# Kernel tuning notes

Hardware: AMD Instinct MI355X
Metric: run time of the kernel (lower is better)

Reference implementation:

```python
import jax, jax.numpy as jnp
import numpy as np

N_NODES = 65536   # entity nodes across batched docs
N_EDGES = 32768   # edges per etype
D_CTX = 768       # PTM hidden size ('n' feature)
D_REL = 97        # relation_num (out_feature)
CHUNK = 1024      # edge chunk for the per-edge bilinear


def setup_inputs() -> dict:
    key = jax.random.key(0)
    ks = jax.random.split(key, 10)
    n = jax.random.normal(ks[0], (N_NODES, D_CTX), jnp.float32)
    e_inter = jax.random.normal(ks[1], (N_EDGES, D_REL), jnp.float32)
    e_intra = jax.random.normal(ks[2], (N_EDGES, D_REL), jnp.float32)
    # nn.Bilinear(768, 97, 1, bias=False): weight [1, 768, 97]
    W_bl = jax.random.normal(ks[3], (1, D_CTX, D_REL), jnp.float32) * 0.02
    # nn.Bilinear(194, 194, 97): weight [97, 194, 194], bias [97]
    W_bl1 = jax.random.normal(ks[4], (D_REL, 2 * D_REL, 2 * D_REL), jnp.float32) * 0.02
    b_bl1 = jnp.zeros((D_REL,), jnp.float32)
    src_inter = jax.random.randint(ks[5], (N_EDGES,), 0, N_NODES, jnp.int32)
    dst_inter = jax.random.randint(ks[6], (N_EDGES,), 0, N_NODES, jnp.int32)
    src_intra = jax.random.randint(ks[7], (N_EDGES,), 0, N_NODES, jnp.int32)
    dst_intra = jax.random.randint(ks[8], (N_EDGES,), 0, N_NODES, jnp.int32)
    return {"n": n, "e_inter": e_inter, "e_intra": e_intra,
            "W_bl": W_bl, "W_bl1": W_bl1, "b_bl1": b_bl1,
            "src_inter": src_inter, "dst_inter": dst_inter,
            "src_intra": src_intra, "dst_intra": dst_intra}


def reference(n, e_inter, e_intra, W_bl, W_bl1, b_bl1,
              src_inter, dst_inter, src_intra, dst_intra):
    num_nodes = n.shape[0]
    # node_reduce: score = bilinear(n[dst], e) -> softmax over incoming edges
    # bl(src_n, e) = n[dst] @ W_bl[0] @ e  (precompute node projection once)
    proj = n @ W_bl[0]                                  # [N, D_REL]

    def node_reduce(e, dst):
        s = jnp.sum(proj[dst] * e, axis=-1)             # per-edge score [E]
        smax = jax.ops.segment_max(s, dst, num_segments=num_nodes)
        ex = jnp.exp(s - smax[dst])
        denom = jax.ops.segment_sum(ex, dst, num_segments=num_nodes)
        alpha = ex / denom[dst]                          # segment softmax
        # attention-weighted sum of mailbox messages -> [N, D_REL]
        return jax.ops.segment_sum(e * alpha[:, None], dst, num_segments=num_nodes)

    # multi_update_all(..., 'stack') over etypes ['inter','intra'] then flatten
    rel = jnp.concatenate([node_reduce(e_inter, dst_inter),
                           node_reduce(e_intra, dst_intra)], axis=-1)  # [N, 194]

    def edge_gate(e, src, dst):
        s_rel = rel[src]                                 # [E, 194]
        d_rel = rel[dst]                                 # [E, 194]
        d_in = s_rel.shape[1]

        def f(args):
            s, d = args                                  # [CHUNK, 194]
            return jnp.einsum('ei,kij,ej->ek', s, W_bl1, d, optimize=True) + b_bl1

        gate = jax.lax.map(f, (s_rel.reshape(-1, CHUNK, d_in),
                               d_rel.reshape(-1, CHUNK, d_in)))
        gate = gate.reshape(e.shape[0], -1)              # [E, D_REL]
        return e + jax.nn.sigmoid(gate) * e

    out_inter = edge_gate(e_inter, src_inter, dst_inter)
    out_intra = edge_gate(e_intra, src_intra, dst_intra)
    return jnp.stack([out_inter, out_intra])             # [2, E, D_REL]
```

## Files before the change

kernel.cpp:

```cpp
#include <hip/hip_runtime.h>
#include <hip/hip_bf16.h>
#include <stdint.h>


typedef __attribute__((ext_vector_type(8))) short short8;
typedef __attribute__((ext_vector_type(4))) float f32x4;
typedef _Float16 half8 __attribute__((ext_vector_type(8)));

#define NN 65536
#define NE1 32768
#define NEG 65536
#define DC 768
#define DR 97
#define DR2 194
#define RELSTR 200
#define RELHS 400
#define KI 194
#define KS 7
#define NT 7
#define EPB 64
#define SSTR 200
#define PSTR 72
#define NDESC_G 4160

#define OFF_REL   0ull
#define OFF_BPK   52428800ull
#define OFF_IDX   62164992ull
#define OFF_SMAX  62427136ull
#define OFF_DEN   62951424ull
#define OFF_META  63475712ull
#define OFF_DESC  63475968ull
#define OFF_WPK   63542528ull

static __device__ __forceinline__ unsigned fkey(float f) {
    unsigned b = __float_as_uint(f);
    return (b & 0x80000000u) ? ~b : (b | 0x80000000u);
}
static __device__ __forceinline__ float funkey(unsigned k) {
    return __uint_as_float((k & 0x80000000u) ? (k & 0x7fffffffu) : ~k);
}
static __device__ __forceinline__ unsigned pk2(_Float16 a, _Float16 b) {
    union { _Float16 h[2]; unsigned u; } x;
    x.h[0] = a; x.h[1] = b;
    return x.u;
}
static __device__ __forceinline__ int nstate(bool zi, bool zx) {
    return zi ? (zx ? 3 : 2) : (zx ? 1 : 0);
}
static __device__ __forceinline__ int nsplit_of(int b) { (void)b; return 4; }
static __device__ __forceinline__ int kindbase_of(int b) { return (b % 3) * 4; }

__global__ void build_bpk(const float* __restrict__ W, half8* __restrict__ Bpk) {
    int id = blockIdx.x * blockDim.x + threadIdx.x;
    const int total = KI * KS * NT * 64;
    if (id >= total) return;
    int l = id & 63;
    int g = id >> 6;
    int t = g % NT;
    int ks = (g / NT) % KS;
    int i = g / (NT * KS);
    int kk = t * 16 + (l & 15);
    int jb = ks * 32 + (l >> 4) * 8;
    half8 pk;
#pragma unroll
    for (int m = 0; m < 8; ++m) {
        int j = jb + m;
        float f = (kk < DR && j < DR2) ? W[(size_t)kk * (DR2 * DR2) + i * DR2 + j] : 0.f;
        pk[m] = (_Float16)f;
    }
    Bpk[id] = pk;
}

__global__ void build_wpk(const float* __restrict__ Wb, half8* __restrict__ Wpk) {
    int id = blockIdx.x * blockDim.x + threadIdx.x;
    const int total = 24 * NT * 64;
    if (id >= total) return;
    int l = id & 63;
    int g = id >> 6;
    int t = g % NT;
    int k2 = g / NT;
    int col = t * 16 + (l & 15);
    int j0 = k2 * 32 + (l >> 4) * 8;
    half8 pk;
#pragma unroll
    for (int m = 0; m < 8; ++m) {
        float f = (col < DR) ? Wb[(size_t)(j0 + m) * DR + col] : 0.f;
        pk[m] = (_Float16)f;
    }
    Wpk[id] = pk;
}

__launch_bounds__(512, 8)
__global__ void proj_mfma(const float* __restrict__ nmat, const half8* __restrict__ Wpk,
                          float* __restrict__ proj) {
    __shared__ __align__(16) _Float16 a_lds[128][PSTR];
    int tid = threadIdx.x;
    int r0 = blockIdx.x << 7;
    int w = tid >> 6, lane = tid & 63;
    int er = (w << 4) + (lane & 15);
    int lk = lane >> 4;

    f32x4 acc[NT];
#pragma unroll
    for (int t = 0; t < NT; ++t) acc[t] = (f32x4){0.f, 0.f, 0.f, 0.f};

    int srow = tid >> 2;
    int sc0 = (tid & 3) << 4;
    const float* nrow = nmat + (size_t)(r0 + srow) * DC + sc0;

    for (int k0 = 0; k0 < DC; k0 += 64) {
        __syncthreads();
        {
            const f32x4* p = (const f32x4*)(nrow + k0);
            _Float16* dst = &a_lds[srow][sc0];
#pragma unroll
            for (int q = 0; q < 4; ++q) {
                f32x4 v = p[q];
                *(unsigned*)&dst[q * 4]     = pk2((_Float16)v[0], (_Float16)v[1]);
                *(unsigned*)&dst[q * 4 + 2] = pk2((_Float16)v[2], (_Float16)v[3]);
            }
        }
        __syncthreads();
#pragma unroll
        for (int kk = 0; kk < 2; ++kk) {
            half8 af = *(const half8*)&a_lds[er][kk * 32 + lk * 8];
            const half8* bp = Wpk + (size_t)((k0 >> 5) + kk) * (NT * 64) + lane;
#pragma unroll
            for (int t = 0; t < NT; ++t)
                acc[t] = __builtin_amdgcn_mfma_f32_16x16x32_f16(af, bp[t * 64], acc[t], 0, 0, 0);
        }
    }

#pragma unroll
    for (int t = 0; t < NT; ++t) {
        int col = t * 16 + (lane & 15);
        if (col < DR) {
#pragma unroll
            for (int r = 0; r < 4; ++r) {
                int row = r0 + (w << 4) + lk * 4 + r;
                proj[(size_t)row * DR + col] = acc[t][r];
            }
        }
    }
}

__global__ void score_kernel(const float* __restrict__ proj,
                             const float* __restrict__ e_inter, const float* __restrict__ e_intra,
                             const int* __restrict__ dst_inter, const int* __restrict__ dst_intra,
                             float* __restrict__ s_buf, unsigned* __restrict__ smax_key) {
    int wid = (blockIdx.x * blockDim.x + threadIdx.x) >> 6;
    int lane = threadIdx.x & 63;
    if (wid >= NEG) return;
    int et = wid >> 15, le = wid & (NE1 - 1);
    const float* e = (et ? e_intra : e_inter) + (size_t)le * DR;
    int dst = (et ? dst_intra : dst_inter)[le];
    const float* pr = proj + (size_t)dst * DR;
    float p = pr[lane] * e[lane];
    if (lane < DR - 64) p += pr[lane + 64] * e[lane + 64];
#pragma unroll
    for (int off = 32; off > 0; off >>= 1) p += __shfl_down(p, off);
    if (lane == 0) {
        s_buf[wid] = p;
        atomicMax(&smax_key[et * NN + dst], fkey(p));
    }
}

__global__ void accum_kernel(const float* __restrict__ s_buf,
                             const float* __restrict__ e_inter, const float* __restrict__ e_intra,
                             const int* __restrict__ dst_inter, const int* __restrict__ dst_intra,
                             const unsigned* __restrict__ smax_key,
                             float* __restrict__ denom, float* __restrict__ rel) {
    int wid = (blockIdx.x * blockDim.x + threadIdx.x) >> 6;
    int lane = threadIdx.x & 63;
    if (wid >= NEG) return;
    int et = wid >> 15, le = wid & (NE1 - 1);
    const float* e = (et ? e_intra : e_inter) + (size_t)le * DR;
    int dst = (et ? dst_intra : dst_inter)[le];
    float s = s_buf[wid];
    float mx = funkey(smax_key[et * NN + dst]);
    float ex = __expf(s - mx);
    if (lane == 0) atomicAdd(&denom[et * NN + dst], ex);
    float* rrow = rel + (size_t)dst * RELSTR + et * DR;
    atomicAdd(&rrow[lane], e[lane] * ex);
    if (lane < DR - 64) atomicAdd(&rrow[lane + 64], e[lane + 64] * ex);
}

__global__ void dinv_kernel(float* __restrict__ denom) {
    int i = blockIdx.x * blockDim.x + threadIdx.x;
    if (i < 2 * NN) {
        float d = denom[i];
        denom[i] = (d > 0.f) ? (1.f / d) : 0.f;
    }
}

__global__ void pack_kernel(float* __restrict__ relf, const float* __restrict__ dinv) {
    int n = blockIdx.x * blockDim.x + threadIdx.x;
    if (n >= NN) return;
    float di0 = dinv[n], di1 = dinv[NN + n];
    unsigned* row = (unsigned*)(relf + (size_t)n * RELSTR);
#pragma unroll 10
    for (int q = 0; q < 50; ++q) {
        uint4 v = *(const uint4*)(row + q * 4);
        int c = q * 4;
        _Float16 h0 = (_Float16)(__uint_as_float(v.x) * ((c + 0 < DR) ? di0 : di1));
        _Float16 h1 = (_Float16)(__uint_as_float(v.y) * ((c + 1 < DR) ? di0 : di1));
        _Float16 h2 = (_Float16)(__uint_as_float(v.z) * ((c + 2 < DR) ? di0 : di1));
        _Float16 h3 = (_Float16)(__uint_as_float(v.w) * ((c + 3 < DR) ? di0 : di1));
        uint2 o;
        o.x = pk2(h0, h1);
        o.y = pk2(h2, h3);
        *(uint2*)(row + q * 2) = o;
    }
}

__global__ void classify_kernel(const float* __restrict__ dinv,
                                const int* __restrict__ src_inter, const int* __restrict__ dst_inter,
                                const int* __restrict__ src_intra, const int* __restrict__ dst_intra,
                                unsigned* __restrict__ meta) {
    __shared__ unsigned h[16];
    if (threadIdx.x < 16) h[threadIdx.x] = 0;
    __syncthreads();
    int gid = blockIdx.x * blockDim.x + threadIdx.x;
    if (gid < NEG) {
        int et = gid >> 15, le = gid & (NE1 - 1);
        int sn = (et ? src_intra : src_inter)[le];
        int dn = (et ? dst_intra : dst_inter)[le];
        int ss = nstate(dinv[sn] == 0.f, dinv[NN + sn] == 0.f);
        int ds = nstate(dinv[dn] == 0.f, dinv[NN + dn] == 0.f);
        int b = (ss == 3 || ds == 3) ? 9 : ss * 3 + ds;
        atomicAdd(&h[b], 1u);
    }
    __syncthreads();
    if (threadIdx.x < 10 && h[threadIdx.x])
        atomicAdd(&meta[threadIdx.x], h[threadIdx.x]);
}

__global__ void setup1_kernel(unsigned* __restrict__ meta) {
    if (threadIdx.x != 0 || blockIdx.x != 0) return;
    unsigned run = 0;
    for (int b = 0; b < 10; ++b) {
        meta[32 + b] = run;
        meta[16 + b] = run;
        run += meta[b];
    }
    unsigned c = 0;
    for (int b = 0; b < 9; ++b) {
        meta[52 + b] = c;
        c += ((meta[b] + EPB - 1) / EPB) * (unsigned)nsplit_of(b);
    }
    meta[48] = c;
}

__global__ void setup2_kernel(const unsigned* __restrict__ meta, uint4* __restrict__ desc) {
    int j = blockIdx.x * blockDim.x + threadIdx.x;
    if (j >= (int)meta[48]) return;
    int b = 8;
    for (int q = 1; q < 9; ++q)
        if (j < (int)meta[52 + q]) { b = q - 1; break; }
    int p = j - (int)meta[52 + b];
    int ns = nsplit_of(b);
    int ci = p / ns;
    int si = p - ci * ns;
    int cnt = (int)meta[b];
    int cbase = (int)meta[32 + b] + ci * EPB;
    int ccnt = cnt - ci * EPB;
    if (ccnt > EPB) ccnt = EPB;
    int kind = kindbase_of(b) + si;
    int sclass = b / 3;
    desc[j] = make_uint4((unsigned)kind, (unsigned)cbase, (unsigned)ccnt, (unsigned)sclass);
}

__global__ void scatter_kernel(const float* __restrict__ dinv,
                               const int* __restrict__ src_inter, const int* __restrict__ dst_inter,
                               const int* __restrict__ src_intra, const int* __restrict__ dst_intra,
                               unsigned* __restrict__ meta, int* __restrict__ idxbuf) {
    __shared__ unsigned cur[16];
    __shared__ unsigned base[16];
    if (threadIdx.x < 16) cur[threadIdx.x] = 0;
    __syncthreads();
    int gid = blockIdx.x * blockDim.x + threadIdx.x;
    int b = -1;
    unsigned r = 0;
    if (gid < NEG) {
        int et = gid >> 15, le = gid & (NE1 - 1);
        int sn = (et ? src_intra : src_inter)[le];
        int dn = (et ? dst_intra : dst_inter)[le];
        int ss = nstate(dinv[sn] == 0.f, dinv[NN + sn] == 0.f);
        int ds = nstate(dinv[dn] == 0.f, dinv[NN + dn] == 0.f);
        b = (ss == 3 || ds == 3) ? 9 : ss * 3 + ds;
        r = atomicAdd(&cur[b], 1u);
    }
    __syncthreads();
    if (threadIdx.x < 10 && cur[threadIdx.x])
        base[threadIdx.x] = atomicAdd(&meta[16 + threadIdx.x], cur[threadIdx.x]);
    __syncthreads();
    if (b >= 0) idxbuf[base[b] + r] = gid;
}

__global__ void skip_kernel(const unsigned* __restrict__ meta, const int* __restrict__ idxbuf,
                            const float* __restrict__ e_inter, const float* __restrict__ e_intra,
                            const float* __restrict__ bias, float* __restrict__ out) {
    int n9 = (int)meta[9];
    int base9 = (int)meta[41];
    int k = threadIdx.x;
    float g = 0.f;
    if (k < DR) {
        float b = bias[k];
        g = 1.f + 1.f / (1.f + __expf(-b));
    }
    for (int q = blockIdx.x; q < n9; q += gridDim.x) {
        int gid = idxbuf[base9 + q];
        int et = gid >> 15, le = gid & (NE1 - 1);
        const float* e = (et ? e_intra : e_inter) + (size_t)le * DR;
        if (k < DR) out[(size_t)gid * DR + k] = e[k] * g;
    }
}

#define GATE_BODY(KS0v, KS1v, T0v, T1v)                                        \
    {                                                                          \
        constexpr int NKSv = (KS1v) - (KS0v);                                  \
        constexpr int NTTv = (T1v) - (T0v);                                    \
        f32x4 acc0[NTTv], acc1[NTTv];                                          \
        _Pragma("unroll")                                                      \
        for (int tt = 0; tt < NTTv; ++tt) {                                    \
            acc0[tt] = (f32x4){0.f, 0.f, 0.f, 0.f};                            \
            acc1[tt] = (f32x4){0.f, 0.f, 0.f, 0.f};                            \
        }                                                                      \
        const half8* bl = Bpk + lane;                                          \
        for (int i = i0; i < iEnd; ++i) {                                      \
            _Float16 s0 = buf[er0 * SSTR + i];                                 \
            _Float16 s1 = buf[er1 * SSTR + i];                                 \
            half8 sv0 = {s0, s0, s0, s0, s0, s0, s0, s0};                      \
            half8 sv1 = {s1, s1, s1, s1, s1, s1, s1, s1};                      \
            const half8* bi = bl + (size_t)((i * KS + (KS0v)) * NT + (T0v)) * 64; \
            _Pragma("unroll")                                                  \
            for (int ks = 0; ks < NKSv; ++ks) {                                \
                half8 af0 = sv0 * dv0[(KS0v) + ks];                            \
                half8 af1 = sv1 * dv1[(KS0v) + ks];                            \
                _Pragma("unroll")                                              \
                for (int tt = 0; tt < NTTv; ++tt) {                            \
                    half8 bv = bi[(ks * NT + tt) * 64];                        \
                    acc0[tt] = __builtin_amdgcn_mfma_f32_16x16x32_f16(af0, bv, acc0[tt], 0, 0, 0); \
                    acc1[tt] = __builtin_amdgcn_mfma_f32_16x16x32_f16(af1, bv, acc1[tt], 0, 0, 0); \
                }                                                              \
            }                                                                  \
        }                                                                      \
        _Pragma("unroll")                                                      \
        for (int r = 0; r < 4; ++r) {                                          \
            int row = (w << 5) + lk * 4 + r;                                   \
            if (row < ccnt) {                                                  \
                int gid = idxbuf[cbase + row];                                 \
                int et = gid >> 15, le = gid & (NE1 - 1);                      \
                const float* e = (et ? e_intra : e_inter) + (size_t)le * DR;   \
                float* o = out + (size_t)gid * DR;                             \
                _Pragma("unroll")                                              \
                for (int tt = 0; tt < NTTv; ++tt) {                            \
                    int k = ((T0v) + tt) * 16 + (lane & 15);                   \
                    if (k < DR) {                                              \
                        float g = acc0[tt][r] + bias[k];                       \
                        float sg = 1.f / (1.f + __expf(-g));                   \
                        o[k] = e[k] * (1.f + sg);                              \
                    }                                                          \
                }                                                              \
            }                                                                  \
        }                                                                      \
        _Pragma("unroll")                                                      \
        for (int r = 0; r < 4; ++r) {                                          \
            int row = (w << 5) + 16 + lk * 4 + r;                              \
            if (row < ccnt) {                                                  \
                int gid = idxbuf[cbase + row];                                 \
                int et = gid >> 15, le = gid & (NE1 - 1);                      \
                const float* e = (et ? e_intra : e_inter) + (size_t)le * DR;   \
                float* o = out + (size_t)gid * DR;                             \
                _Pragma("unroll")                                              \
                for (int tt = 0; tt < NTTv; ++tt) {                            \
                    int k = ((T0v) + tt) * 16 + (lane & 15);                   \
                    if (k < DR) {                                              \
                        float g = acc1[tt][r] + bias[k];                       \
                        float sg = 1.f / (1.f + __expf(-g));                   \
                        o[k] = e[k] * (1.f + sg);                              \
                    }                                                          \
                }                                                              \
            }                                                                  \
        }                                                                      \
    }

__launch_bounds__(128, 4)
__global__ void gate_all(const _Float16* __restrict__ relh, const float* __restrict__ dinv,
                         const half8* __restrict__ Bpk, const float* __restrict__ bias,
                         const int* __restrict__ src_inter, const int* __restrict__ dst_inter,
                         const int* __restrict__ src_intra, const int* __restrict__ dst_intra,
                         const float* __restrict__ e_inter, const float* __restrict__ e_intra,
                         const int* __restrict__ idxbuf, const unsigned* __restrict__ meta,
                         const uint4* __restrict__ desc, float* __restrict__ out) {
    if (blockIdx.x >= meta[48]) return;
    uint4 de = desc[blockIdx.x];
    int kind = (int)de.x;
    int cbase = (int)de.y;
    int ccnt = (int)de.z;
    int sclass = (int)de.w;
    int i0 = (sclass == 2) ? DR : 0;
    int iEnd = (sclass == 0) ? DR2 : (i0 + DR);

    __shared__ __align__(16) _Float16 buf[EPB * SSTR];
    int tid = threadIdx.x;
    int w = tid >> 6;
    int lane = tid & 63;
    int lk = lane >> 4;
    int er0 = (w << 5) + (lane & 15);
    int er1 = er0 + 16;

    if (tid < EPB) {
        int edge = tid;
        int rc = cbase + ((edge < ccnt) ? edge : (ccnt - 1));
        int gid = idxbuf[rc];
        int et = gid >> 15, le = gid & (NE1 - 1);
        int dn = (et ? dst_intra : dst_inter)[le];
        const uint4* rp = (const uint4*)(relh + (size_t)dn * RELHS);
        uint4* dp = (uint4*)&buf[edge * SSTR];
#pragma unroll
        for (int q = 0; q < 25; ++q) dp[q] = rp[q];
    }
    __syncthreads();

    half8 dv0[KS], dv1[KS];
#pragma unroll
    for (int ks = 0; ks < KS; ++ks) {
        if (ks == 6 && lk > 0) {
            dv0[ks] = (half8){0, 0, 0, 0, 0, 0, 0, 0};
            dv1[ks] = (half8){0, 0, 0, 0, 0, 0, 0, 0};
        } else {
            dv0[ks] = *(const half8*)&buf[er0 * SSTR + ks * 32 + lk * 8];
            dv1[ks] = *(const half8*)&buf[er1 * SSTR + ks * 32 + lk * 8];
        }
    }
    __syncthreads();

    if (tid < EPB) {
        int edge = tid;
        int rc = cbase + ((edge < ccnt) ? edge : (ccnt - 1));
        int gid = idxbuf[rc];
        int et = gid >> 15, le = gid & (NE1 - 1);
        int sn = (et ? src_intra : src_inter)[le];
        const uint4* rp = (const uint4*)(relh + (size_t)sn * RELHS);
        uint4* dp = (uint4*)&buf[edge * SSTR];
#pragma unroll
        for (int q = 0; q < 25; ++q) dp[q] = rp[q];
    }
    __syncthreads();

    switch (kind) {
        case 0:  GATE_BODY(0, 7, 0, 2); break;
        case 1:  GATE_BODY(0, 7, 2, 4); break;
        case 2:  GATE_BODY(0, 7, 4, 6); break;
        case 3:  GATE_BODY(0, 7, 6, 7); break;
        case 4:  GATE_BODY(0, 4, 0, 2); break;
        case 5:  GATE_BODY(0, 4, 2, 4); break;
        case 6:  GATE_BODY(0, 4, 4, 6); break;
        case 7:  GATE_BODY(0, 4, 6, 7); break;
        case 8:  GATE_BODY(3, 7, 0, 2); break;
        case 9:  GATE_BODY(3, 7, 2, 4); break;
        case 10: GATE_BODY(3, 7, 4, 6); break;
        case 11: GATE_BODY(3, 7, 6, 7); break;
        default: break;
    }
}

extern "C" void kernel_launch(void* const* d_in, const int* in_sizes, int n_in,
                              void* d_out, int out_size, void* d_ws, size_t ws_size,
                              hipStream_t stream) {
    (void)in_sizes; (void)n_in; (void)out_size; (void)ws_size;
    const float* nmat     = (const float*)d_in[0];
    const float* e_inter  = (const float*)d_in[1];
    const float* e_intra  = (const float*)d_in[2];
    const float* W_bl     = (const float*)d_in[3];
    const float* W_bl1    = (const float*)d_in[4];
    const float* b_bl1    = (const float*)d_in[5];
    const int* src_inter  = (const int*)d_in[6];
    const int* dst_inter  = (const int*)d_in[7];
    const int* src_intra  = (const int*)d_in[8];
    const int* dst_intra  = (const int*)d_in[9];
    float* out = (float*)d_out;

    char* ws = (char*)d_ws;
    float* regA     = (float*)(ws + OFF_REL);
    half8* Bpk      = (half8*)(ws + OFF_BPK);
    int* idxbuf     = (int*)(ws + OFF_IDX);
    float* s_buf    = (float*)(ws + OFF_IDX);
    unsigned* smax  = (unsigned*)(ws + OFF_SMAX);
    float* denom    = (float*)(ws + OFF_DEN);
    unsigned* meta  = (unsigned*)(ws + OFF_META);
    uint4* desc     = (uint4*)(ws + OFF_DESC);
    half8* Wpk      = (half8*)(ws + OFF_WPK);

    hipMemsetAsync(smax, 0, 524288, stream);
    hipMemsetAsync(denom, 0, 524288, stream);
    hipMemsetAsync(meta, 0, 256, stream);

    build_bpk<<<(KI * KS * NT * 64 + 255) / 256, 256, 0, stream>>>(W_bl1, Bpk);
    build_wpk<<<(24 * NT * 64 + 255) / 256, 256, 0, stream>>>(W_bl, Wpk);
    proj_mfma<<<NN / 128, 512, 0, stream>>>(nmat, Wpk, regA);
    score_kernel<<<NEG / 4, 256, 0, stream>>>(regA, e_inter, e_intra, dst_inter, dst_intra,
                                              s_buf, smax);
    hipMemsetAsync(regA, 0, 52428800, stream);
    accum_kernel<<<NEG / 4, 256, 0, stream>>>(s_buf, e_inter, e_intra, dst_inter, dst_intra,
                                              smax, denom, regA);
    dinv_kernel<<<512, 256, 0, stream>>>(denom);
    pack_kernel<<<NN / 256, 256, 0, stream>>>(regA, denom);
    classify_kernel<<<NEG / 256, 256, 0, stream>>>(denom, src_inter, dst_inter,
                                                   src_intra, dst_intra, meta);
    setup1_kernel<<<1, 64, 0, stream>>>(meta);
    setup2_kernel<<<(NDESC_G + 255) / 256, 256, 0, stream>>>(meta, desc);
    scatter_kernel<<<NEG / 256, 256, 0, stream>>>(denom, src_inter, dst_inter,
                                                  src_intra, dst_intra, meta, idxbuf);
    skip_kernel<<<2048, 128, 0, stream>>>(meta, idxbuf, e_inter, e_intra, b_bl1, out);
    gate_all<<<NDESC_G, 128, 0, stream>>>((const _Float16*)regA, denom, Bpk, b_bl1,
                                          src_inter, dst_inter, src_intra, dst_intra,
                                          e_inter, e_intra, idxbuf, meta, desc, out);
}
```

Measured before the change: 538.5 us.

## Use single-wave gate blocks covering all 64 edges to double B-fragment reuse

The gate kernel now runs one 64-lane wave per block instead of two. That wave handles all 64 edges of the tile with four accumulator sets, so each packed W_bl1 fragment loaded from global memory feeds four MFMAs instead of two. The aim is to halve B-operand traffic per edge. The cost is twice the accumulator and dst-vector registers per thread, and fewer waves per block to hide latency.

```diff
diff --git a/kernel.cpp b/kernel.cpp
--- a/kernel.cpp
+++ b/kernel.cpp
@@ -316,76 +316,74 @@
     }
 }
 
+#define EPI_SUB(ACC, AOFF)                                                     \
+    _Pragma("unroll")                                                          \
+    for (int r = 0; r < 4; ++r) {                                              \
+        int row = (AOFF) + lk * 4 + r;                                         \
+        if (row < ccnt) {                                                      \
+            int gid = idxbuf[cbase + row];                                     \
+            int et = gid >> 15, le = gid & (NE1 - 1);                          \
+            const float* e = (et ? e_intra : e_inter) + (size_t)le * DR;       \
+            float* o = out + (size_t)gid * DR;                                 \
+            _Pragma("unroll")                                                  \
+            for (int tt = 0; tt < NTTv; ++tt) {                                \
+                int k = (T0c + tt) * 16 + (lane & 15);                         \
+                if (k < DR) {                                                  \
+                    float g = ACC[tt][r] + bias[k];                            \
+                    float sg = 1.f / (1.f + __expf(-g));                       \
+                    o[k] = e[k] * (1.f + sg);                                  \
+                }                                                              \
+            }                                                                  \
+        }                                                                      \
+    }
+
 #define GATE_BODY(KS0v, KS1v, T0v, T1v)                                        \
     {                                                                          \
         constexpr int NKSv = (KS1v) - (KS0v);                                  \
         constexpr int NTTv = (T1v) - (T0v);                                    \
-        f32x4 acc0[NTTv], acc1[NTTv];                                          \
+        constexpr int T0c = (T0v);                                             \
+        f32x4 acc0[NTTv], acc1[NTTv], acc2[NTTv], acc3[NTTv];                  \
         _Pragma("unroll")                                                      \
         for (int tt = 0; tt < NTTv; ++tt) {                                    \
             acc0[tt] = (f32x4){0.f, 0.f, 0.f, 0.f};                            \
             acc1[tt] = (f32x4){0.f, 0.f, 0.f, 0.f};                            \
+            acc2[tt] = (f32x4){0.f, 0.f, 0.f, 0.f};                            \
+            acc3[tt] = (f32x4){0.f, 0.f, 0.f, 0.f};                            \
         }                                                                      \
         const half8* bl = Bpk + lane;                                          \
         for (int i = i0; i < iEnd; ++i) {                                      \
             _Float16 s0 = buf[er0 * SSTR + i];                                 \
             _Float16 s1 = buf[er1 * SSTR + i];                                 \
+            _Float16 s2 = buf[er2 * SSTR + i];                                 \
+            _Float16 s3 = buf[er3 * SSTR + i];                                 \
             half8 sv0 = {s0, s0, s0, s0, s0, s0, s0, s0};                      \
             half8 sv1 = {s1, s1, s1, s1, s1, s1, s1, s1};                      \
+            half8 sv2 = {s2, s2, s2, s2, s2, s2, s2, s2};                      \
+            half8 sv3 = {s3, s3, s3, s3, s3, s3, s3, s3};                      \
             const half8* bi = bl + (size_t)((i * KS + (KS0v)) * NT + (T0v)) * 64; \
             _Pragma("unroll")                                                  \
             for (int ks = 0; ks < NKSv; ++ks) {                                \
                 half8 af0 = sv0 * dv0[(KS0v) + ks];                            \
                 half8 af1 = sv1 * dv1[(KS0v) + ks];                            \
+                half8 af2 = sv2 * dv2[(KS0v) + ks];                            \
+                half8 af3 = sv3 * dv3[(KS0v) + ks];                            \
                 _Pragma("unroll")                                              \
                 for (int tt = 0; tt < NTTv; ++tt) {                            \
                     half8 bv = bi[(ks * NT + tt) * 64];                        \
                     acc0[tt] = __builtin_amdgcn_mfma_f32_16x16x32_f16(af0, bv, acc0[tt], 0, 0, 0); \
                     acc1[tt] = __builtin_amdgcn_mfma_f32_16x16x32_f16(af1, bv, acc1[tt], 0, 0, 0); \
+                    acc2[tt] = __builtin_amdgcn_mfma_f32_16x16x32_f16(af2, bv, acc2[tt], 0, 0, 0); \
+                    acc3[tt] = __builtin_amdgcn_mfma_f32_16x16x32_f16(af3, bv, acc3[tt], 0, 0, 0); \
                 }                                                              \
             }                                                                  \
         }                                                                      \
-        _Pragma("unroll")                                                      \
-        for (int r = 0; r < 4; ++r) {                                          \
-            int row = (w << 5) + lk * 4 + r;                                   \
-            if (row < ccnt) {                                                  \
-                int gid = idxbuf[cbase + row];                                 \
-                int et = gid >> 15, le = gid & (NE1 - 1);                      \
-                const float* e = (et ? e_intra : e_inter) + (size_t)le * DR;   \
-                float* o = out + (size_t)gid * DR;                             \
-                _Pragma("unroll")                                              \
-                for (int tt = 0; tt < NTTv; ++tt) {                            \
-                    int k = ((T0v) + tt) * 16 + (lane & 15);                   \
-                    if (k < DR) {                                              \
-                        float g = acc0[tt][r] + bias[k];                       \
-                        float sg = 1.f / (1.f + __expf(-g));                   \
-                        o[k] = e[k] * (1.f + sg);                              \
-                    }                                                          \
-                }                                                              \
-            }                                                                  \
-        }                                                                      \
-        _Pragma("unroll")                                                      \
-        for (int r = 0; r < 4; ++r) {                                          \
-            int row = (w << 5) + 16 + lk * 4 + r;                              \
-            if (row < ccnt) {                                                  \
-                int gid = idxbuf[cbase + row];                                 \
-                int et = gid >> 15, le = gid & (NE1 - 1);                      \
-                const float* e = (et ? e_intra : e_inter) + (size_t)le * DR;   \
-                float* o = out + (size_t)gid * DR;                             \
-                _Pragma("unroll")                                              \
-                for (int tt = 0; tt < NTTv; ++tt) {                            \
-                    int k = ((T0v) + tt) * 16 + (lane & 15);                   \
-                    if (k < DR) {                                              \
-                        float g = acc1[tt][r] + bias[k];                       \
-                        float sg = 1.f / (1.f + __expf(-g));                   \
-                        o[k] = e[k] * (1.f + sg);                              \
-                    }                                                          \
-                }                                                              \
-            }                                                                  \
-        }                                                                      \
-    }
-
-__launch_bounds__(128, 4)
+        EPI_SUB(acc0, 0)                                                       \
+        EPI_SUB(acc1, 16)                                                      \
+        EPI_SUB(acc2, 32)                                                      \
+        EPI_SUB(acc3, 48)                                                      \
+    }
+
+__launch_bounds__(64, 2)
 __global__ void gate_all(const _Float16* __restrict__ relh, const float* __restrict__ dinv,
                          const half8* __restrict__ Bpk, const float* __restrict__ bias,
                          const int* __restrict__ src_inter, const int* __restrict__ dst_inter,
@@ -404,13 +402,14 @@
 
     __shared__ __align__(16) _Float16 buf[EPB * SSTR];
     int tid = threadIdx.x;
-    int w = tid >> 6;
-    int lane = tid & 63;
+    int lane = tid;
     int lk = lane >> 4;
-    int er0 = (w << 5) + (lane & 15);
+    int er0 = lane & 15;
     int er1 = er0 + 16;
-
-    if (tid < EPB) {
+    int er2 = er0 + 32;
+    int er3 = er0 + 48;
+
+    {
         int edge = tid;
         int rc = cbase + ((edge < ccnt) ? edge : (ccnt - 1));
         int gid = idxbuf[rc];
@@ -423,20 +422,24 @@
     }
     __syncthreads();
 
-    half8 dv0[KS], dv1[KS];
+    half8 dv0[KS], dv1[KS], dv2[KS], dv3[KS];
 #pragma unroll
     for (int ks = 0; ks < KS; ++ks) {
         if (ks == 6 && lk > 0) {
             dv0[ks] = (half8){0, 0, 0, 0, 0, 0, 0, 0};
             dv1[ks] = (half8){0, 0, 0, 0, 0, 0, 0, 0};
+            dv2[ks] = (half8){0, 0, 0, 0, 0, 0, 0, 0};
+            dv3[ks] = (half8){0, 0, 0, 0, 0, 0, 0, 0};
         } else {
             dv0[ks] = *(const half8*)&buf[er0 * SSTR + ks * 32 + lk * 8];
             dv1[ks] = *(const half8*)&buf[er1 * SSTR + ks * 32 + lk * 8];
+            dv2[ks] = *(const half8*)&buf[er2 * SSTR + ks * 32 + lk * 8];
+            dv3[ks] = *(const half8*)&buf[er3 * SSTR + ks * 32 + lk * 8];
         }
     }
     __syncthreads();
 
-    if (tid < EPB) {
+    {
         int edge = tid;
         int rc = cbase + ((edge < ccnt) ? edge : (ccnt - 1));
         int gid = idxbuf[rc];
@@ -514,7 +517,7 @@
     scatter_kernel<<<NEG / 256, 256, 0, stream>>>(denom, src_inter, dst_inter,
                                                   src_intra, dst_intra, meta, idxbuf);
     skip_kernel<<<2048, 128, 0, stream>>>(meta, idxbuf, e_inter, e_intra, b_bl1, out);
-    gate_all<<<NDESC_G, 128, 0, stream>>>((const _Float16*)regA, denom, Bpk, b_bl1,
-                                          src_inter, dst_inter, src_intra, dst_intra,
-                                          e_inter, e_intra, idxbuf, meta, desc, out);
-}
+    gate_all<<<NDESC_G, 64, 0, stream>>>((const _Float16*)regA, denom, Bpk, b_bl1,
+                                         src_inter, dst_inter, src_intra, dst_intra,
+                                         e_inter, e_intra, idxbuf, meta, desc, out);
+}
```

Result: slower. 801.2 us (+48.8%).
